# Performance work log

Measured on AMD Instinct MI355X. Metric: run time of the kernel, lower is better.

The kernel has to match this reference:

```python
import jax, jax.numpy as jnp
import numpy as np

B, CIN, HIN, WIN = 1, 26, 721, 1440
K, HOUT, KH, KW = 9, 360, 9, 9
COUT = 256
PSCALE = WIN // (WIN // 2)  # lon downsample stride = 2
WOUT = WIN // 2


def setup_inputs() -> dict:
    key = jax.random.key(0)
    k1, k2, k3 = jax.random.split(key, 3)
    x = jax.random.normal(k1, (B, CIN, HIN, WIN), dtype=jnp.float32)
    # precomputed basis*quadrature stencil psi[k, ho, dh, dw] (shift-invariant in lon,
    # stored only for wo=0, exactly as DISCO does). Normalized per (k, ho) ('mean' mode).
    psi = jax.random.normal(k2, (K, HOUT, KH, KW), dtype=jnp.float32)
    psi = psi / (jnp.mean(jnp.abs(psi), axis=(2, 3), keepdims=True) * (KH * KW) + 1e-6)
    weight = jax.random.normal(k3, (COUT, CIN, K), dtype=jnp.float32) * (1.0 / np.sqrt(CIN * K))
    # base input-lat row for each output lat (stencil top row), clipped to valid range
    hi_base = np.clip(np.round(np.arange(HOUT) * (HIN - 1) / HOUT).astype(np.int32) - KH // 2, 0, HIN - 1)
    return {"x": x, "psi": psi, "weight": weight, "hi_base": jnp.asarray(hi_base, dtype=jnp.int32)}


def _disco_conv(x, psi, weight, hi_base):
    x = x.astype(jnp.float32)  # fp32 autocast-off region, matches torch module
    acc = jnp.zeros((B, CIN, K, HOUT, WOUT), dtype=jnp.float32)
    for dh in range(KH):  # small structural loop over stencil rows
        rows = jnp.clip(hi_base + dh, 0, HIN - 1)  # [Hout]
        xr = x[:, :, rows, :]
        for dw in range(KW):  # small structural loop over stencil lon offsets
            shift = dw - KW // 2
            xs = jnp.roll(xr, -shift, axis=-1)[..., ::PSCALE]  # [B,C,Hout,Wout]
            acc = acc + psi[:, :, dh, dw][None, None, :, :, None] * xs[:, :, None, :, :]
    # contract learned weights over kernel basis and input channels
    out = jnp.einsum('bckhw,ock->bohw', acc, weight)  # [B,Cout,Hout,Wout]
    return out


def reference(x, psi, weight, hi_base):
    return _disco_conv(x, psi, weight, hi_base)
```

## Files before the change

kernel.cpp:

```cpp
#include <hip/hip_runtime.h>
#include <hip/hip_bf16.h>

#define CIN_   26
#define HIN_   721
#define WIN_   1440
#define K_     9
#define HOUT_  360
#define KH_    9
#define KW_    9
#define COUT_  256
#define WOUT_  720

#define WT     16
#define XSP    48
#define CCH    7
#define CK     (CIN_ * K_)
#define NKS2   9
#define ACCP2  296
#define NMT    (COUT_ / 16)
#define NXCD   8
#define HBAND  (HOUT_ / NXCD)

typedef short bf16x8 __attribute__((ext_vector_type(8)));
typedef float f32x4  __attribute__((ext_vector_type(4)));

__device__ unsigned short g_whi[NMT * NKS2 * 64 * 8];
__device__ unsigned short g_pfrag[HOUT_ * 3 * 64 * 8];

__device__ __forceinline__ unsigned short f2bf_rne(float f) {
    union { float f; unsigned u; } v; v.f = f;
    unsigned u = v.u;
    unsigned r = (u + 0x7FFFu + ((u >> 16) & 1u)) >> 16;
    return (unsigned short)r;
}
__device__ __forceinline__ unsigned pack_bf2(float a, float b) {
    const __hip_bfloat162 bv = __float22bfloat162_rn(make_float2(a, b));
    return *reinterpret_cast<const unsigned*>(&bv);
}

__global__ void prep_weight_kernel(const float* __restrict__ weight) {
    const int bid  = blockIdx.x;
    const int mt   = bid / NKS2;
    const int ks   = bid % NKS2;
    const int lane = threadIdx.x;
    const int row  = mt * 16 + (lane & 15);
    const int k0   = ks * 32 + (lane >> 4) * 8;
    const int base = ((mt * NKS2 + ks) * 64 + lane) * 8;
    #pragma unroll
    for (int j = 0; j < 8; ++j) {
        const int kp = k0 + j;
        float w = 0.f;
        if (kp < 260) {
            const int c = kp / 10, m = kp % 10;
            if (m < 9) w = weight[row * CK + c * 9 + m];
        }
        g_whi[base + j] = f2bf_rne(w);
    }
}

__global__ void prep_psi_kernel(const float* __restrict__ psi) {
    const int h    = blockIdx.x;
    const int lane = threadIdx.x;
    const int m    = lane & 15;
    const int kg   = lane >> 4;
    #pragma unroll
    for (int ks = 0; ks < 3; ++ks) {
        const int base = ((h * 3 + ks) * 64 + lane) * 8;
        #pragma unroll
        for (int e = 0; e < 8; ++e) {
            const int s = ks * 32 + kg * 8 + e;
            float v = 0.f;
            if (m < 9) {
                if (s < 72)      v = psi[(m * HOUT_ + h) * 81 + (s >> 3) * 9 + (s & 7)];
                else if (s < 81) v = psi[(m * HOUT_ + h) * 81 + (s - 72) * 9 + 8];
            }
            g_pfrag[base + e] = f2bf_rne(v);
        }
    }
}

#define LDS_BARRIER()                                      \
    do {                                                   \
        asm volatile("s_waitcnt lgkmcnt(0)" ::: "memory"); \
        __builtin_amdgcn_s_barrier();                      \
    } while (0)

__global__ __launch_bounds__(256, 6)
void disco_fused_kernel(const float* __restrict__ x,
                        const int*   __restrict__ hi_base,
                        float* __restrict__ out)
{
    __shared__ unsigned short xs_bf[2][CCH * KH_][XSP];
    __shared__ __align__(16) unsigned short acc_s[WT][ACCP2];

    const int b    = blockIdx.x;
    const int xcd  = b & (NXCD - 1);
    const int jb   = b >> 3;
    const int h    = xcd * HBAND + jb / 45;
    const int tile = jb % 45;
    const int w0   = tile * WT;
    const int tid  = threadIdx.x;

    const int hib = hi_base[h];

    #pragma unroll
    for (int t = 0; t < 2; ++t) {
        const int e = tid + t * 256;
        if (e < 16 * 28) acc_s[e / 28][260 + e % 28] = 0;
    }

    const int lane = tid & 63;
    const int wid  = tid >> 6;
    const int n    = lane & 15;
    const int kg   = lane >> 4;

    bf16x8 afrag[3];
    #pragma unroll
    for (int ks = 0; ks < 3; ++ks)
        afrag[ks] = *(const bf16x8*)&g_pfrag[((h * 3 + ks) * 64 + lane) * 8];

    const int c0 = 2 * w0 - 4;

    #define ISSUE(RD, V, S)                                                          \
    do {                                                                             \
        const int items = ((RD) == 3) ? 450 : 630;                                   \
        _Pragma("unroll")                                                            \
        for (int t = 0; t < 3; ++t) {                                                \
            const int i  = tid + t * 256;                                            \
            const int ii = (i < items) ? i : (items - 1);                            \
            const int q  = ii % 10;                                                  \
            const int lr = ii / 10;                                                  \
            const int dh = lr % 9;                                                   \
            const int c  = (RD) * CCH + lr / 9;                                      \
            int r = hib + dh;                                                        \
            if (r > HIN_ - 1) r = HIN_ - 1;                                          \
            int g = c0 + 4 * q;                                                      \
            if (g < 0)          g += WIN_;                                           \
            else if (g >= WIN_) g -= WIN_;                                           \
            V[t] = *reinterpret_cast<const float4*>(                                 \
                x + ((size_t)c * HIN_ + r) * WIN_ + g);                              \
            S[t] = (i < items) ? (lr * XSP + 4 * q) : -1;                            \
        }                                                                            \
    } while (0)

    #define WRITE(RD, V, S)                                                          \
    do {                                                                             \
        unsigned short* dst = &xs_bf[(RD) & 1][0][0];                                \
        _Pragma("unroll")                                                            \
        for (int t = 0; t < 3; ++t) {                                                \
            if (S[t] >= 0) {                                                         \
                uint2 dv;                                                            \
                dv.x = pack_bf2(V[t].x, V[t].y);                                     \
                dv.y = pack_bf2(V[t].z, V[t].w);                                     \
                *reinterpret_cast<uint2*>(dst + S[t]) = dv;                          \
            }                                                                        \
        }                                                                            \
    } while (0)

    float4 va[3], vb[3];
    int    sa[3], sb[3];

    ISSUE(0, va, sa);
    WRITE(0, va, sa);
    ISSUE(1, vb, sb);
    LDS_BARRIER();

    #pragma unroll
    for (int rd = 0; rd < 4; ++rd) {
        const int nc = (rd == 3) ? (CIN_ - 3 * CCH) : CCH;
        const char* xsb = (const char*)&xs_bf[rd & 1][0][0];

        for (int cc = wid; cc < nc; cc += 4) {
            const int c    = rd * CCH + cc;
            const int base = cc * (KH_ * XSP * 2) + 4 * n;
            f32x4 C = {0.f, 0.f, 0.f, 0.f};
            #pragma unroll
            for (int ks = 0; ks < 3; ++ks) {
                union { bf16x8 v; unsigned d[4]; unsigned short u[8]; } bf;
                if (ks < 2 || kg == 0) {
                    const char* p = xsb + base + (ks * 4 + kg) * (XSP * 2);
                    #pragma unroll
                    for (int t = 0; t < 4; ++t)
                        bf.d[t] = *(const unsigned*)(p + 4 * t);
                } else if (kg == 1) {
                    #pragma unroll
                    for (int e = 0; e < 8; ++e)
                        bf.u[e] = *(const unsigned short*)(xsb + base + e * (XSP * 2) + 16);
                } else if (kg == 2) {
                    bf.d[0] = bf.d[1] = bf.d[2] = bf.d[3] = 0;
                    bf.u[0] = *(const unsigned short*)(xsb + base + 8 * (XSP * 2) + 16);
                } else {
                    bf.d[0] = bf.d[1] = bf.d[2] = bf.d[3] = 0;
                }
                C = __builtin_amdgcn_mfma_f32_16x16x32_bf16(afrag[ks], bf.v, C, 0, 0, 0);
            }
            if (kg < 2) {
                unsigned* ap = reinterpret_cast<unsigned*>(&acc_s[n][c * 10 + kg * 4]);
                ap[0] = pack_bf2(C[0], C[1]);
                ap[1] = pack_bf2(C[2], C[3]);
            } else if (kg == 2) {
                *reinterpret_cast<unsigned*>(&acc_s[n][c * 10 + 8]) = pack_bf2(C[0], 0.f);
            }
        }

        if (rd == 0)      { WRITE(1, vb, sb); ISSUE(2, va, sa); }
        else if (rd == 1) { WRITE(2, va, sa); ISSUE(3, vb, sb); }
        else if (rd == 2) { WRITE(3, vb, sb); }
        LDS_BARRIER();
    }
    #undef ISSUE
    #undef WRITE

    f32x4 C0 = {0.f, 0.f, 0.f, 0.f};
    f32x4 C1 = C0, C2 = C0, C3 = C0;

    const unsigned short* wp = g_whi + ((size_t)(wid * 4) * NKS2 * 64 + lane) * 8;

    bf16x8 wc[4];
    #pragma unroll
    for (int i = 0; i < 4; ++i)
        wc[i] = *(const bf16x8*)(wp + (size_t)i * NKS2 * 512);

    #pragma unroll
    for (int ks = 0; ks < NKS2; ++ks) {
        bf16x8 wn[4];
        if (ks + 1 < NKS2) {
            #pragma unroll
            for (int i = 0; i < 4; ++i)
                wn[i] = *(const bf16x8*)(wp + ((size_t)i * NKS2 + (ks + 1)) * 512);
        }
        const bf16x8 bhi = *(const bf16x8*)&acc_s[n][ks * 32 + kg * 8];
        C0 = __builtin_amdgcn_mfma_f32_16x16x32_bf16(wc[0], bhi, C0, 0, 0, 0);
        C1 = __builtin_amdgcn_mfma_f32_16x16x32_bf16(wc[1], bhi, C1, 0, 0, 0);
        C2 = __builtin_amdgcn_mfma_f32_16x16x32_bf16(wc[2], bhi, C2, 0, 0, 0);
        C3 = __builtin_amdgcn_mfma_f32_16x16x32_bf16(wc[3], bhi, C3, 0, 0, 0);
        if (ks + 1 < NKS2) {
            #pragma unroll
            for (int i = 0; i < 4; ++i) wc[i] = wn[i];
        }
    }

    #pragma unroll
    for (int i = 0; i < 4; ++i) {
        const f32x4 acc = (i == 0) ? C0 : (i == 1) ? C1 : (i == 2) ? C2 : C3;
        const int m0 = (wid * 4 + i) * 16 + kg * 4;
        #pragma unroll
        for (int r = 0; r < 4; ++r) {
            out[(size_t)(m0 + r) * (HOUT_ * WOUT_) + h * WOUT_ + w0 + n] = acc[r];
        }
    }
}

extern "C" void kernel_launch(void* const* d_in, const int* in_sizes, int n_in,
                              void* d_out, int out_size, void* d_ws, size_t ws_size,
                              hipStream_t stream)
{
    const float* x       = (const float*)d_in[0];
    const float* psi     = (const float*)d_in[1];
    const float* weight  = (const float*)d_in[2];
    const int*   hi_base = (const int*)d_in[3];
    float* out = (float*)d_out;

    hipLaunchKernelGGL(prep_weight_kernel, dim3(NMT * NKS2), dim3(64), 0, stream, weight);
    hipLaunchKernelGGL(prep_psi_kernel,    dim3(HOUT_),      dim3(64), 0, stream, psi);

    dim3 grid(45 * HOUT_, 1, 1);
    dim3 block(256, 1, 1);
    hipLaunchKernelGGL(disco_fused_kernel, grid, block, 0, stream,
                       x, hi_base, out);
}
```

Before: 256.9 us.

## Warp-specialize fused kernel into producer and consumer waves across five tiles

Each block now handles five consecutive longitude tiles of one output row with 512 threads. Four producer waves load and convert input, then compute the psi stencil MFMA into a double-buffered LDS accumulator. Four consumer waves run the channel-mixing GEMM and store output for the previous tile, so the two stages of adjacent tiles overlap. This uses more LDS and registers per block and adds a pipeline fill and drain step per block.

```diff
diff --git a/kernel.cpp b/kernel.cpp
--- a/kernel.cpp
+++ b/kernel.cpp
@@ -19,7 +19,7 @@
 #define ACCP2  296
 #define NMT    (COUT_ / 16)
 #define NXCD   8
-#define HBAND  (HOUT_ / NXCD)
+#define TW     5
 
 typedef short bf16x8 __attribute__((ext_vector_type(8)));
 typedef float f32x4  __attribute__((ext_vector_type(4)));
@@ -85,48 +85,52 @@
         __builtin_amdgcn_s_barrier();                      \
     } while (0)
 
-__global__ __launch_bounds__(256, 6)
+__global__ __launch_bounds__(512, 4)
 void disco_fused_kernel(const float* __restrict__ x,
                         const int*   __restrict__ hi_base,
                         float* __restrict__ out)
 {
     __shared__ unsigned short xs_bf[2][CCH * KH_][XSP];
-    __shared__ __align__(16) unsigned short acc_s[WT][ACCP2];
-
-    const int b    = blockIdx.x;
-    const int xcd  = b & (NXCD - 1);
-    const int jb   = b >> 3;
-    const int h    = xcd * HBAND + jb / 45;
-    const int tile = jb % 45;
-    const int w0   = tile * WT;
-    const int tid  = threadIdx.x;
+    __shared__ __align__(16) unsigned short acc_s[2][WT][ACCP2];
+
+    const int b     = blockIdx.x;
+    const int xcd   = b & (NXCD - 1);
+    const int g     = b >> 3;
+    const int h     = xcd * 45 + g / 9;
+    const int tile0 = (g % 9) * TW;
+    const int tid   = threadIdx.x;
 
     const int hib = hi_base[h];
-
-    #pragma unroll
-    for (int t = 0; t < 2; ++t) {
-        const int e = tid + t * 256;
-        if (e < 16 * 28) acc_s[e / 28][260 + e % 28] = 0;
+    const bool producer = (tid < 256);
+
+    if (tid < 2 * 16 * 14) {
+        const int p  = tid / 224;
+        const int r2 = tid % 224;
+        *reinterpret_cast<unsigned*>(&acc_s[p][r2 / 14][260 + 2 * (r2 % 14)]) = 0u;
     }
 
     const int lane = tid & 63;
-    const int wid  = tid >> 6;
+    const int widp = tid >> 6;
     const int n    = lane & 15;
     const int kg   = lane >> 4;
 
     bf16x8 afrag[3];
-    #pragma unroll
-    for (int ks = 0; ks < 3; ++ks)
-        afrag[ks] = *(const bf16x8*)&g_pfrag[((h * 3 + ks) * 64 + lane) * 8];
-
-    const int c0 = 2 * w0 - 4;
-
-    #define ISSUE(RD, V, S)                                                          \
+    if (producer) {
+        #pragma unroll
+        for (int ks = 0; ks < 3; ++ks)
+            afrag[ks] = *(const bf16x8*)&g_pfrag[((h * 3 + ks) * 64 + lane) * 8];
+    }
+
+    const int wid2 = widp - 4;
+    const unsigned short* wp = g_whi +
+        ((size_t)(((widp & 3) * 4)) * NKS2 * 64 + lane) * 8;
+
+    #define ISSUE(RD, C0V, V, S)                                                     \
     do {                                                                             \
         const int items = ((RD) == 3) ? 450 : 630;                                   \
         _Pragma("unroll")                                                            \
-        for (int t = 0; t < 3; ++t) {                                                \
-            const int i  = tid + t * 256;                                            \
+        for (int t_ = 0; t_ < 3; ++t_) {                                             \
+            const int i  = tid + t_ * 256;                                           \
             const int ii = (i < items) ? i : (items - 1);                            \
             const int q  = ii % 10;                                                  \
             const int lr = ii / 10;                                                  \
@@ -134,12 +138,12 @@
             const int c  = (RD) * CCH + lr / 9;                                      \
             int r = hib + dh;                                                        \
             if (r > HIN_ - 1) r = HIN_ - 1;                                          \
-            int g = c0 + 4 * q;                                                      \
-            if (g < 0)          g += WIN_;                                           \
-            else if (g >= WIN_) g -= WIN_;                                           \
-            V[t] = *reinterpret_cast<const float4*>(                                 \
-                x + ((size_t)c * HIN_ + r) * WIN_ + g);                              \
-            S[t] = (i < items) ? (lr * XSP + 4 * q) : -1;                            \
+            int gg = (C0V) + 4 * q;                                                  \
+            if (gg < 0)          gg += WIN_;                                         \
+            else if (gg >= WIN_) gg -= WIN_;                                         \
+            V[t_] = *reinterpret_cast<const float4*>(                                \
+                x + ((size_t)c * HIN_ + r) * WIN_ + gg);                             \
+            S[t_] = (i < items) ? (lr * XSP + 4 * q) : -1;                           \
         }                                                                            \
     } while (0)
 
@@ -147,12 +151,12 @@
     do {                                                                             \
         unsigned short* dst = &xs_bf[(RD) & 1][0][0];                                \
         _Pragma("unroll")                                                            \
-        for (int t = 0; t < 3; ++t) {                                                \
-            if (S[t] >= 0) {                                                         \
+        for (int t_ = 0; t_ < 3; ++t_) {                                             \
+            if (S[t_] >= 0) {                                                        \
                 uint2 dv;                                                            \
-                dv.x = pack_bf2(V[t].x, V[t].y);                                     \
-                dv.y = pack_bf2(V[t].z, V[t].w);                                     \
-                *reinterpret_cast<uint2*>(dst + S[t]) = dv;                          \
+                dv.x = pack_bf2(V[t_].x, V[t_].y);                                   \
+                dv.y = pack_bf2(V[t_].z, V[t_].w);                                   \
+                *reinterpret_cast<uint2*>(dst + S[t_]) = dv;                         \
             }                                                                        \
         }                                                                            \
     } while (0)
@@ -160,95 +164,109 @@
     float4 va[3], vb[3];
     int    sa[3], sb[3];
 
-    ISSUE(0, va, sa);
-    WRITE(0, va, sa);
-    ISSUE(1, vb, sb);
-    LDS_BARRIER();
-
-    #pragma unroll
-    for (int rd = 0; rd < 4; ++rd) {
-        const int nc = (rd == 3) ? (CIN_ - 3 * CCH) : CCH;
-        const char* xsb = (const char*)&xs_bf[rd & 1][0][0];
-
-        for (int cc = wid; cc < nc; cc += 4) {
-            const int c    = rd * CCH + cc;
-            const int base = cc * (KH_ * XSP * 2) + 4 * n;
-            f32x4 C = {0.f, 0.f, 0.f, 0.f};
+    f32x4 C0 = {0.f, 0.f, 0.f, 0.f}, C1 = C0, C2 = C0, C3 = C0;
+    bf16x8 wc[4];
+
+    for (int t = 0; t <= TW; ++t) {
+        const bool prod_act = producer && (t < TW);
+        const bool cons_act = (!producer) && (t > 0);
+        const int  c0p = 2 * ((tile0 + t) * WT) - 4;
+        const int  qb  = (t - 1) & 1;
+
+        if (prod_act) {
+            ISSUE(0, c0p, va, sa);
+            WRITE(0, va, sa);
+            ISSUE(1, c0p, vb, sb);
+        }
+        if (cons_act) {
+            C0 = (f32x4){0.f, 0.f, 0.f, 0.f}; C1 = C0; C2 = C0; C3 = C0;
             #pragma unroll
-            for (int ks = 0; ks < 3; ++ks) {
-                union { bf16x8 v; unsigned d[4]; unsigned short u[8]; } bf;
-                if (ks < 2 || kg == 0) {
-                    const char* p = xsb + base + (ks * 4 + kg) * (XSP * 2);
+            for (int i = 0; i < 4; ++i)
+                wc[i] = *(const bf16x8*)(wp + (size_t)i * NKS2 * 512);
+        }
+        LDS_BARRIER();
+
+        #pragma unroll
+        for (int rd = 0; rd < 4; ++rd) {
+            if (prod_act) {
+                const int nc = (rd == 3) ? (CIN_ - 3 * CCH) : CCH;
+                const char* xsb = (const char*)&xs_bf[rd & 1][0][0];
+                for (int cc = widp; cc < nc; cc += 4) {
+                    const int c    = rd * CCH + cc;
+                    const int base = cc * (KH_ * XSP * 2) + 4 * n;
+                    f32x4 Cp = {0.f, 0.f, 0.f, 0.f};
                     #pragma unroll
-                    for (int t = 0; t < 4; ++t)
-                        bf.d[t] = *(const unsigned*)(p + 4 * t);
-                } else if (kg == 1) {
+                    for (int ks = 0; ks < 3; ++ks) {
+                        union { bf16x8 v; unsigned d[4]; unsigned short u[8]; } bf;
+                        if (ks < 2 || kg == 0) {
+                            const char* p = xsb + base + (ks * 4 + kg) * (XSP * 2);
+                            #pragma unroll
+                            for (int t_ = 0; t_ < 4; ++t_)
+                                bf.d[t_] = *(const unsigned*)(p + 4 * t_);
+                        } else if (kg == 1) {
+                            #pragma unroll
+                            for (int e = 0; e < 8; ++e)
+                                bf.u[e] = *(const unsigned short*)(xsb + base + e * (XSP * 2) + 16);
+                        } else if (kg == 2) {
+                            bf.d[0] = bf.d[1] = bf.d[2] = bf.d[3] = 0;
+                            bf.u[0] = *(const unsigned short*)(xsb + base + 8 * (XSP * 2) + 16);
+                        } else {
+                            bf.d[0] = bf.d[1] = bf.d[2] = bf.d[3] = 0;
+                        }
+                        Cp = __builtin_amdgcn_mfma_f32_16x16x32_bf16(afrag[ks], bf.v, Cp, 0, 0, 0);
+                    }
+                    if (kg < 2) {
+                        unsigned* ap = reinterpret_cast<unsigned*>(&acc_s[t & 1][n][c * 10 + kg * 4]);
+                        ap[0] = pack_bf2(Cp[0], Cp[1]);
+                        ap[1] = pack_bf2(Cp[2], Cp[3]);
+                    } else if (kg == 2) {
+                        *reinterpret_cast<unsigned*>(&acc_s[t & 1][n][c * 10 + 8]) = pack_bf2(Cp[0], 0.f);
+                    }
+                }
+                if (rd == 0)      { WRITE(1, vb, sb); ISSUE(2, c0p, va, sa); }
+                else if (rd == 1) { WRITE(2, va, sa); ISSUE(3, c0p, vb, sb); }
+                else if (rd == 2) { WRITE(3, vb, sb); }
+            }
+
+            if (cons_act) {
+                if (rd < 3) {
                     #pragma unroll
-                    for (int e = 0; e < 8; ++e)
-                        bf.u[e] = *(const unsigned short*)(xsb + base + e * (XSP * 2) + 16);
-                } else if (kg == 2) {
-                    bf.d[0] = bf.d[1] = bf.d[2] = bf.d[3] = 0;
-                    bf.u[0] = *(const unsigned short*)(xsb + base + 8 * (XSP * 2) + 16);
+                    for (int kq = 0; kq < 3; ++kq) {
+                        const int ks = rd * 3 + kq;
+                        bf16x8 wn[4];
+                        if (ks + 1 < NKS2) {
+                            #pragma unroll
+                            for (int i = 0; i < 4; ++i)
+                                wn[i] = *(const bf16x8*)(wp + ((size_t)i * NKS2 + (ks + 1)) * 512);
+                        }
+                        const bf16x8 bq = *(const bf16x8*)&acc_s[qb][n][ks * 32 + kg * 8];
+                        C0 = __builtin_amdgcn_mfma_f32_16x16x32_bf16(wc[0], bq, C0, 0, 0, 0);
+                        C1 = __builtin_amdgcn_mfma_f32_16x16x32_bf16(wc[1], bq, C1, 0, 0, 0);
+                        C2 = __builtin_amdgcn_mfma_f32_16x16x32_bf16(wc[2], bq, C2, 0, 0, 0);
+                        C3 = __builtin_amdgcn_mfma_f32_16x16x32_bf16(wc[3], bq, C3, 0, 0, 0);
+                        if (ks + 1 < NKS2) {
+                            #pragma unroll
+                            for (int i = 0; i < 4; ++i) wc[i] = wn[i];
+                        }
+                    }
                 } else {
-                    bf.d[0] = bf.d[1] = bf.d[2] = bf.d[3] = 0;
+                    const int w0c = (tile0 + t - 1) * WT;
+                    #pragma unroll
+                    for (int i = 0; i < 4; ++i) {
+                        const f32x4 acc = (i == 0) ? C0 : (i == 1) ? C1 : (i == 2) ? C2 : C3;
+                        const int m0 = (wid2 * 4 + i) * 16 + kg * 4;
+                        #pragma unroll
+                        for (int r = 0; r < 4; ++r) {
+                            out[(size_t)(m0 + r) * (HOUT_ * WOUT_) + h * WOUT_ + w0c + n] = acc[r];
+                        }
+                    }
                 }
-                C = __builtin_amdgcn_mfma_f32_16x16x32_bf16(afrag[ks], bf.v, C, 0, 0, 0);
             }
-            if (kg < 2) {
-                unsigned* ap = reinterpret_cast<unsigned*>(&acc_s[n][c * 10 + kg * 4]);
-                ap[0] = pack_bf2(C[0], C[1]);
-                ap[1] = pack_bf2(C[2], C[3]);
-            } else if (kg == 2) {
-                *reinterpret_cast<unsigned*>(&acc_s[n][c * 10 + 8]) = pack_bf2(C[0], 0.f);
-            }
-        }
-
-        if (rd == 0)      { WRITE(1, vb, sb); ISSUE(2, va, sa); }
-        else if (rd == 1) { WRITE(2, va, sa); ISSUE(3, vb, sb); }
-        else if (rd == 2) { WRITE(3, vb, sb); }
-        LDS_BARRIER();
+            LDS_BARRIER();
+        }
     }
     #undef ISSUE
     #undef WRITE
-
-    f32x4 C0 = {0.f, 0.f, 0.f, 0.f};
-    f32x4 C1 = C0, C2 = C0, C3 = C0;
-
-    const unsigned short* wp = g_whi + ((size_t)(wid * 4) * NKS2 * 64 + lane) * 8;
-
-    bf16x8 wc[4];
-    #pragma unroll
-    for (int i = 0; i < 4; ++i)
-        wc[i] = *(const bf16x8*)(wp + (size_t)i * NKS2 * 512);
-
-    #pragma unroll
-    for (int ks = 0; ks < NKS2; ++ks) {
-        bf16x8 wn[4];
-        if (ks + 1 < NKS2) {
-            #pragma unroll
-            for (int i = 0; i < 4; ++i)
-                wn[i] = *(const bf16x8*)(wp + ((size_t)i * NKS2 + (ks + 1)) * 512);
-        }
-        const bf16x8 bhi = *(const bf16x8*)&acc_s[n][ks * 32 + kg * 8];
-        C0 = __builtin_amdgcn_mfma_f32_16x16x32_bf16(wc[0], bhi, C0, 0, 0, 0);
-        C1 = __builtin_amdgcn_mfma_f32_16x16x32_bf16(wc[1], bhi, C1, 0, 0, 0);
-        C2 = __builtin_amdgcn_mfma_f32_16x16x32_bf16(wc[2], bhi, C2, 0, 0, 0);
-        C3 = __builtin_amdgcn_mfma_f32_16x16x32_bf16(wc[3], bhi, C3, 0, 0, 0);
-        if (ks + 1 < NKS2) {
-            #pragma unroll
-            for (int i = 0; i < 4; ++i) wc[i] = wn[i];
-        }
-    }
-
-    #pragma unroll
-    for (int i = 0; i < 4; ++i) {
-        const f32x4 acc = (i == 0) ? C0 : (i == 1) ? C1 : (i == 2) ? C2 : C3;
-        const int m0 = (wid * 4 + i) * 16 + kg * 4;
-        #pragma unroll
-        for (int r = 0; r < 4; ++r) {
-            out[(size_t)(m0 + r) * (HOUT_ * WOUT_) + h * WOUT_ + w0 + n] = acc[r];
-        }
-    }
 }
 
 extern "C" void kernel_launch(void* const* d_in, const int* in_sizes, int n_in,
@@ -264,8 +282,8 @@
     hipLaunchKernelGGL(prep_weight_kernel, dim3(NMT * NKS2), dim3(64), 0, stream, weight);
     hipLaunchKernelGGL(prep_psi_kernel,    dim3(HOUT_),      dim3(64), 0, stream, psi);
 
-    dim3 grid(45 * HOUT_, 1, 1);
-    dim3 block(256, 1, 1);
+    dim3 grid(3240, 1, 1);
+    dim3 block(512, 1, 1);
     hipLaunchKernelGGL(disco_fused_kernel, grid, block, 0, stream,
                        x, hi_base, out);
 }
```

Result: slower. 913.2 us (+255.5%).
